# Performance work log

Measured on AMD Instinct MI355X. Metric: run time of the kernel, lower is better.

The kernel has to match this reference:

```python
import jax, jax.numpy as jnp
import numpy as np

B, T, C, H = 2, 4096, 512, 8
HD = C // H  # head_dim = 64


def setup_inputs() -> dict:
    key = jax.random.key(0)
    ks = jax.random.split(key, 5)
    s = 0.02
    return {
        "x": jax.random.normal(ks[0], (B, T, C), dtype=jnp.float32),
        "Wqkv": jax.random.normal(ks[1], (C, 3 * C), dtype=jnp.float32) * s,
        "bqkv": jax.random.normal(ks[2], (3 * C,), dtype=jnp.float32) * s,
        "Wproj": jax.random.normal(ks[3], (C, C), dtype=jnp.float32) * s,
        "bproj": jax.random.normal(ks[4], (C,), dtype=jnp.float32) * s,
    }


def reference(x, Wqkv, bqkv, Wproj, bproj):
    b, t, c = x.shape
    qkv = x @ Wqkv + bqkv                      # [B,T,3C]
    q, k, v = jnp.split(qkv, 3, axis=-1)
    # [B,T,C] -> [B,H,T,HD]
    q = q.reshape(b, t, H, HD).transpose(0, 2, 1, 3)
    k = k.reshape(b, t, H, HD).transpose(0, 2, 1, 3)
    v = v.reshape(b, t, H, HD).transpose(0, 2, 1, 3)
    att = jnp.einsum("bhqd,bhkd->bhqk", q, k) / jnp.sqrt(jnp.float32(HD))
    causal = jnp.tril(jnp.ones((t, t), dtype=bool))
    att = jnp.where(causal, att, -jnp.inf)
    att = jax.nn.softmax(att, axis=-1)
    y = jnp.einsum("bhqk,bhkd->bhqd", att, v)  # [B,H,T,HD]
    y = y.transpose(0, 2, 1, 3).reshape(b, t, c)
    return y @ Wproj + bproj
```

## Files before the change

kernel.cpp:

```cpp
#include <hip/hip_runtime.h>
#include <math.h>

#define NB 2
#define NT 4096
#define NC 512
#define NH 8
#define ND 64
#define N3C (3*NC)

typedef __attribute__((ext_vector_type(8))) __bf16 bf16x8;
typedef __attribute__((ext_vector_type(4))) __bf16 bf16x4;
typedef __attribute__((ext_vector_type(4))) float  f32x4;

__device__ __forceinline__ void load_lds16(const __bf16* g, __bf16* l) {
    __builtin_amdgcn_global_load_lds(
        (const __attribute__((address_space(1))) void*)g,
        (__attribute__((address_space(3))) void*)l, 16, 0, 0);
}

__global__ __launch_bounds__(256) void cvt_bf16_kernel(
    const float* __restrict__ x, __bf16* __restrict__ xb, int n)
{
    const int i = (blockIdx.x * 256 + threadIdx.x) << 3;
    if (i < n) {
        float4 a = *(const float4*)(x + i);
        float4 b = *(const float4*)(x + i + 4);
        bf16x8 o;
        o[0] = (__bf16)a.x; o[1] = (__bf16)a.y; o[2] = (__bf16)a.z; o[3] = (__bf16)a.w;
        o[4] = (__bf16)b.x; o[5] = (__bf16)b.y; o[6] = (__bf16)b.z; o[7] = (__bf16)b.w;
        *(bf16x8*)(xb + i) = o;
    }
}

__global__ __launch_bounds__(256) void prep_kernel(
    const float* __restrict__ Wqkv, const float* __restrict__ Wproj,
    __bf16* __restrict__ wqkvt, __bf16* __restrict__ wprojt)
{
    __shared__ float T[64][65];
    int id = blockIdx.x;
    const float* W; __bf16* Wt; int N, n0, k0;
    if (id < 192) { W = Wqkv;  Wt = wqkvt;  N = N3C; n0 = (id % 24) << 6; k0 = (id / 24) << 6; }
    else { id -= 192; W = Wproj; Wt = wprojt; N = NC;  n0 = (id & 7) << 6;  k0 = (id >> 3) << 6; }
    const int K = NC;

    const int tx = threadIdx.x & 15, ty = threadIdx.x >> 4;
#pragma unroll
    for (int i = 0; i < 4; ++i) {
        const int r = ty + (i << 4);
        float4 v = *(const float4*)(W + (size_t)(k0 + r) * N + n0 + (tx << 2));
        T[r][(tx << 2) + 0] = v.x;
        T[r][(tx << 2) + 1] = v.y;
        T[r][(tx << 2) + 2] = v.z;
        T[r][(tx << 2) + 3] = v.w;
    }
    __syncthreads();
#pragma unroll
    for (int i = 0; i < 4; ++i) {
        const int nr = ty + (i << 4);
        bf16x4 o;
        o[0] = (__bf16)T[(tx << 2) + 0][nr];
        o[1] = (__bf16)T[(tx << 2) + 1][nr];
        o[2] = (__bf16)T[(tx << 2) + 2][nr];
        o[3] = (__bf16)T[(tx << 2) + 3][nr];
        *(bf16x4*)(Wt + (size_t)(n0 + nr) * K + k0 + (tx << 2)) = o;
    }
}

template<int BM>
__global__ __launch_bounds__(256) void gemm_glds_kernel(
    const __bf16* __restrict__ A, const __bf16* __restrict__ Bt,
    const float* __restrict__ bias, void* __restrict__ Cout,
    int M, int N, int K, int out_bf16)
{
    constexpr int IT = BM / 32;
    constexpr int AI = BM / 32;
    __shared__ __align__(16) __bf16 As[BM * 64];
    __shared__ __align__(16) __bf16 Bs[128 * 64];

    const int tid  = threadIdx.x;
    const int w    = tid >> 6, lane = tid & 63;
    const int g    = lane >> 4, n = lane & 15;
    const int n7   = n & 7;
    const int wr   = (w >> 1) * (BM / 2);
    const int wc   = (w & 1) << 6;
    const int m0   = blockIdx.y * BM, n0 = blockIdx.x << 7;

    const __bf16* ag[AI]; __bf16* al[AI];
#pragma unroll
    for (int q = 0; q < AI; ++q) {
        const int G = w * (BM * 2) + q * 64 + lane;
        const int r = G >> 3, pg = G & 7, kg = pg ^ (r & 7);
        ag[q] = A + (size_t)(m0 + r) * K + (kg << 3);
        al[q] = As + ((w * (BM * 2) + q * 64) << 3);
    }
    const __bf16* bg[4]; __bf16* bl[4];
#pragma unroll
    for (int q = 0; q < 4; ++q) {
        const int G = w * 256 + q * 64 + lane;
        const int r = G >> 3, pg = G & 7, kg = pg ^ (r & 7);
        bg[q] = Bt + (size_t)(n0 + r) * K + (kg << 3);
        bl[q] = Bs + ((w * 256 + q * 64) << 3);
    }

    f32x4 acc[IT][4];
#pragma unroll
    for (int i = 0; i < IT; ++i)
#pragma unroll
        for (int j = 0; j < 4; ++j) acc[i][j] = (f32x4){0.f, 0.f, 0.f, 0.f};

    const int ksteps = K >> 6;
    for (int ks = 0; ks < ksteps; ++ks) {
        __syncthreads();
        const int ko = ks << 6;
#pragma unroll
        for (int q = 0; q < AI; ++q) load_lds16(ag[q] + ko, al[q]);
#pragma unroll
        for (int q = 0; q < 4;  ++q) load_lds16(bg[q] + ko, bl[q]);
        __syncthreads();

#pragma unroll
        for (int s = 0; s < 2; ++s) {
            bf16x8 af[IT], bf[4];
#pragma unroll
            for (int i = 0; i < IT; ++i) {
                const int row = wr + (i << 4) + n;
                af[i] = *(const bf16x8*)&As[(row << 6) + ((((s << 2) + g) ^ n7) << 3)];
            }
#pragma unroll
            for (int j = 0; j < 4; ++j) {
                const int row = wc + (j << 4) + n;
                bf[j] = *(const bf16x8*)&Bs[(row << 6) + ((((s << 2) + g) ^ n7) << 3)];
            }
#pragma unroll
            for (int i = 0; i < IT; ++i)
#pragma unroll
                for (int j = 0; j < 4; ++j)
                    acc[i][j] = __builtin_amdgcn_mfma_f32_16x16x32_bf16(af[i], bf[j], acc[i][j], 0, 0, 0);
        }
    }

#pragma unroll
    for (int j = 0; j < 4; ++j) {
        const int colg = n0 + wc + (j << 4) + n;
        const float bb = bias[colg];
#pragma unroll
        for (int i = 0; i < IT; ++i) {
#pragma unroll
            for (int reg = 0; reg < 4; ++reg) {
                const int rowg = m0 + wr + (i << 4) + (g << 2) + reg;
                const float v = acc[i][j][reg] + bb;
                if (out_bf16)
                    ((__bf16*)Cout)[(size_t)rowg * N + colg] = (__bf16)v;
                else
                    ((float*)Cout)[(size_t)rowg * N + colg] = v;
            }
        }
    }
}

__global__ __launch_bounds__(512) void attn_kernel(
    const __bf16* __restrict__ qkv, __bf16* __restrict__ out)
{
    __shared__ __align__(16) unsigned char SMEM[36864];
    __bf16 (*QPs)[72] = (__bf16(*)[72])SMEM;
    __bf16 (*Ks)[72]  = (__bf16(*)[72])(SMEM + 18432);
    __bf16 (*Vt)[72]  = (__bf16(*)[72])(SMEM + 27648);

    const int tid  = threadIdx.x;
    const int xi   = blockIdx.x;
    const int bh   = blockIdx.y;
    const int qb   = (bh < 8) ? (31 - xi) : xi;
    const int b    = bh >> 3, h = bh & 7;
    const int qr0  = qb << 7;
    const size_t base = (size_t)b * NT * N3C;
    const int col  = h * ND;

    const int w    = tid >> 6;
    const int lane = tid & 63;
    const int g    = lane >> 4;
    const int n    = lane & 15;
    const int qg   = w >> 1;
    const int kh   = w & 1;
    const int qrow0 = qg << 5;
    const int kcol0 = kh << 5;
    const int sw   = (g ^ (n >> 2)) << 3;

    const int kr = tid >> 3;
    const int kc = (tid & 7) << 3;
    const int vd = lane;
    const int vk = w << 2;

    const __bf16* kptr = qkv + base + NC + col + kc;
    const __bf16* vptr = qkv + base + 2 * NC + col + vd;

#pragma unroll
    for (int i = 0; i < 2; ++i) {
        const int r = kr + (i << 6);
        bf16x8 v = *(const bf16x8*)(qkv + base + (size_t)(qr0 + r) * N3C + col + kc);
        bf16x8 q;
#pragma unroll
        for (int j = 0; j < 8; ++j) q[j] = (__bf16)(0.125f * (float)v[j]);
        *(bf16x8*)&QPs[r][kc] = q;
    }
    __syncthreads();

    bf16x8 qf[2][2];
#pragma unroll
    for (int qt = 0; qt < 2; ++qt)
#pragma unroll
        for (int hh = 0; hh < 2; ++hh)
            qf[qt][hh] = *(const bf16x8*)&QPs[qrow0 + (qt << 4) + n][(hh << 5) + (g << 3)];

    bf16x8 ones;
#pragma unroll
    for (int j = 0; j < 8; ++j) ones[j] = (__bf16)1.0f;

    f32x4 O[2][4];
#pragma unroll
    for (int qt = 0; qt < 2; ++qt)
#pragma unroll
        for (int dt = 0; dt < 4; ++dt) O[qt][dt] = (f32x4){0.f, 0.f, 0.f, 0.f};
    f32x4 L[2] = {{0.f,0.f,0.f,0.f},{0.f,0.f,0.f,0.f}};

    bf16x8 kreg = *(const bf16x8*)(kptr + (size_t)kr * N3C);
    __bf16 vreg[8];
#pragma unroll
    for (int j = 0; j < 4; ++j) {
        vreg[j]     = vptr[(size_t)(vk + j) * N3C];
        vreg[4 + j] = vptr[(size_t)(vk + 32 + j) * N3C];
    }

    const int ntiles = (qb << 1) + 2;
    for (int jt = 0; jt < ntiles; ++jt) {
        __syncthreads();
        *(bf16x8*)&Ks[kr][kc] = kreg;
        {
            bf16x4 va, vb;
#pragma unroll
            for (int j = 0; j < 4; ++j) { va[j] = vreg[j]; vb[j] = vreg[4 + j]; }
            *(bf16x4*)&Vt[vd][vk]      = va;
            *(bf16x4*)&Vt[vd][vk + 32] = vb;
        }
        __syncthreads();

        if (jt + 1 < ntiles) {
            const int kr1 = (jt + 1) << 6;
            kreg = *(const bf16x8*)(kptr + (size_t)(kr1 + kr) * N3C);
#pragma unroll
            for (int j = 0; j < 4; ++j) {
                vreg[j]     = vptr[(size_t)(kr1 + vk + j) * N3C];
                vreg[4 + j] = vptr[(size_t)(kr1 + vk + 32 + j) * N3C];
            }
        }

        f32x4 S[2][2];
        __builtin_amdgcn_s_setprio(1);
#pragma unroll
        for (int t = 0; t < 2; ++t) {
            const bf16x8 k0 = *(const bf16x8*)&Ks[kcol0 + (t << 4) + n][(g << 3)];
            const bf16x8 k1 = *(const bf16x8*)&Ks[kcol0 + (t << 4) + n][32 + (g << 3)];
#pragma unroll
            for (int qt = 0; qt < 2; ++qt) {
                f32x4 a = {0.f, 0.f, 0.f, 0.f};
                a = __builtin_amdgcn_mfma_f32_16x16x32_bf16(qf[qt][0], k0, a, 0, 0, 0);
                a = __builtin_amdgcn_mfma_f32_16x16x32_bf16(qf[qt][1], k1, a, 0, 0, 0);
                S[qt][t] = a;
            }
        }
        __builtin_amdgcn_s_setprio(0);

        if (jt >= (qb << 1)) {
#pragma unroll
            for (int qt = 0; qt < 2; ++qt)
#pragma unroll
                for (int t = 0; t < 2; ++t)
#pragma unroll
                    for (int reg = 0; reg < 4; ++reg) {
                        const int kg = (jt << 6) + kcol0 + (t << 4) + n;
                        const int qgl = qr0 + qrow0 + (qt << 4) + (g << 2) + reg;
                        if (kg > qgl) S[qt][t][reg] = -INFINITY;
                    }
        }

#pragma unroll
        for (int qt = 0; qt < 2; ++qt)
#pragma unroll
            for (int t = 0; t < 2; ++t)
#pragma unroll
                for (int reg = 0; reg < 4; ++reg)
                    QPs[qrow0 + (qt << 4) + (g << 2) + reg]
                       [kcol0 + (((t << 4) + n) ^ (g << 3))] =
                        (__bf16)__expf(S[qt][t][reg]);

        bf16x8 vf[4];
#pragma unroll
        for (int dt = 0; dt < 4; ++dt) {
            const int vr = (dt << 4) + n;
            vf[dt] = *(const bf16x8*)&Vt[vr][kcol0 + (g << 3)];
        }

        __builtin_amdgcn_s_setprio(1);
#pragma unroll
        for (int qt = 0; qt < 2; ++qt) {
            const bf16x8 p = *(const bf16x8*)&QPs[qrow0 + (qt << 4) + n][kcol0 + sw];
            L[qt] = __builtin_amdgcn_mfma_f32_16x16x32_bf16(p, ones, L[qt], 0, 0, 0);
#pragma unroll
            for (int dt = 0; dt < 4; ++dt)
                O[qt][dt] = __builtin_amdgcn_mfma_f32_16x16x32_bf16(p, vf[dt], O[qt][dt], 0, 0, 0);
        }
        __builtin_amdgcn_s_setprio(0);
    }

    __syncthreads();
    float* red = (float*)SMEM;
    if (kh == 1) {
#pragma unroll
        for (int qt = 0; qt < 2; ++qt)
#pragma unroll
            for (int reg = 0; reg < 4; ++reg) {
                const int qlx = qrow0 + (qt << 4) + (g << 2) + reg;
#pragma unroll
                for (int dt = 0; dt < 4; ++dt)
                    red[qlx * 64 + (dt << 4) + n] = O[qt][dt][reg];
                if (n == 0) red[8192 + qlx] = L[qt][reg];
            }
    }
    __syncthreads();
    if (kh == 0) {
#pragma unroll
        for (int qt = 0; qt < 2; ++qt)
#pragma unroll
            for (int reg = 0; reg < 4; ++reg) {
                const int qlx = qrow0 + (qt << 4) + (g << 2) + reg;
                const float inv = 1.0f / (L[qt][reg] + red[8192 + qlx]);
                const size_t row = (size_t)b * NT + qr0 + qlx;
#pragma unroll
                for (int dt = 0; dt < 4; ++dt)
                    out[row * NC + col + (dt << 4) + n] =
                        (__bf16)((O[qt][dt][reg] + red[qlx * 64 + (dt << 4) + n]) * inv);
            }
    }
}

extern "C" void kernel_launch(void* const* d_in, const int* in_sizes, int n_in,
                              void* d_out, int out_size, void* d_ws, size_t ws_size,
                              hipStream_t stream)
{
    const float* x     = (const float*)d_in[0];
    const float* Wqkv  = (const float*)d_in[1];
    const float* bqkv  = (const float*)d_in[2];
    const float* Wproj = (const float*)d_in[3];
    const float* bproj = (const float*)d_in[4];
    float* out = (float*)d_out;

    char* ws = (char*)d_ws;
    __bf16* xb     = (__bf16*)(ws);
    __bf16* qkvb   = (__bf16*)(ws + 8388608);
    __bf16* attb   = (__bf16*)(ws + 33554432);
    __bf16* wqkvt  = (__bf16*)(ws + 41943040);
    __bf16* wprojt = (__bf16*)(ws + 43515904);

    cvt_bf16_kernel<<<dim3(2048), dim3(256), 0, stream>>>(x, xb, NB * NT * NC);
    prep_kernel<<<dim3(256), dim3(256), 0, stream>>>(Wqkv, Wproj, wqkvt, wprojt);

    gemm_glds_kernel<128><<<dim3(N3C / 128, (NB * NT) / 128), dim3(256), 0, stream>>>(
        xb, wqkvt, bqkv, qkvb, NB * NT, N3C, NC, 1);

    attn_kernel<<<dim3(NT / 128, NB * NH), dim3(512), 0, stream>>>(qkvb, attb);

    gemm_glds_kernel<64><<<dim3(NC / 128, (NB * NT) / 64), dim3(256), 0, stream>>>(
        attb, wprojt, bproj, out, NB * NT, NC, NC, 0);
}
```

Measured before the change: 201.7 us.

## Split causal attention KV range across blocks with partial-sum combine kernel

Adds a split-KV (flash-decoding style) path in which later query blocks divide their KV tiles among up to four workgroups. Each workgroup writes unnormalized fp32 partial outputs and row sums, and a new combine kernel adds them and normalizes. The aim is to even out the causal triangle's load imbalance and raise the grid from 512 to 1280 workgroups. In exchange it adds fp32 partial-output traffic (about 40MB of workspace) and one more kernel launch, and it falls back to the single-pass kernel when the workspace is too small.

```diff
diff --git a/kernel.cpp b/kernel.cpp
--- a/kernel.cpp
+++ b/kernel.cpp
@@ -159,7 +159,8 @@
 }
 
 __global__ __launch_bounds__(512) void attn_kernel(
-    const __bf16* __restrict__ qkv, __bf16* __restrict__ out)
+    const __bf16* __restrict__ qkv, int mono, __bf16* __restrict__ outb,
+    float* __restrict__ Opart, float* __restrict__ Lpart)
 {
     __shared__ __align__(16) unsigned char SMEM[36864];
     __bf16 (*QPs)[72] = (__bf16(*)[72])SMEM;
@@ -169,8 +170,25 @@
     const int tid  = threadIdx.x;
     const int xi   = blockIdx.x;
     const int bh   = blockIdx.y;
-    const int qb   = (bh < 8) ? (31 - xi) : xi;
     const int b    = bh >> 3, h = bh & 7;
+
+    int qb, jt0, jt1, pid;
+    if (mono) {
+        qb = (bh < 8) ? (31 - xi) : xi;
+        jt0 = 0; jt1 = (qb << 1) + 2; pid = 0;
+    } else {
+        const int a  = (xi < 8) ? 0 : ((xi < 24) ? 1 : ((xi < 48) ? 2 : 3));
+        const int np = a + 1;
+        const int off = xi - 4 * a * np;
+        qb = (a << 3) + off / np;
+        const int p  = off % np;
+        const int ntiles = (qb << 1) + 2;
+        const int chunk = ntiles / np, rem = ntiles % np;
+        jt0 = p * chunk + (p < rem ? p : rem);
+        jt1 = jt0 + chunk + (p < rem ? 1 : 0);
+        pid = bh * 80 + xi;
+    }
+
     const int qr0  = qb << 7;
     const size_t base = (size_t)b * NT * N3C;
     const int col  = h * ND;
@@ -222,16 +240,16 @@
         for (int dt = 0; dt < 4; ++dt) O[qt][dt] = (f32x4){0.f, 0.f, 0.f, 0.f};
     f32x4 L[2] = {{0.f,0.f,0.f,0.f},{0.f,0.f,0.f,0.f}};
 
-    bf16x8 kreg = *(const bf16x8*)(kptr + (size_t)kr * N3C);
+    const int r0 = jt0 << 6;
+    bf16x8 kreg = *(const bf16x8*)(kptr + (size_t)(r0 + kr) * N3C);
     __bf16 vreg[8];
 #pragma unroll
     for (int j = 0; j < 4; ++j) {
-        vreg[j]     = vptr[(size_t)(vk + j) * N3C];
-        vreg[4 + j] = vptr[(size_t)(vk + 32 + j) * N3C];
-    }
-
-    const int ntiles = (qb << 1) + 2;
-    for (int jt = 0; jt < ntiles; ++jt) {
+        vreg[j]     = vptr[(size_t)(r0 + vk + j) * N3C];
+        vreg[4 + j] = vptr[(size_t)(r0 + vk + 32 + j) * N3C];
+    }
+
+    for (int jt = jt0; jt < jt1; ++jt) {
         __syncthreads();
         *(bf16x8*)&Ks[kr][kc] = kreg;
         {
@@ -243,7 +261,7 @@
         }
         __syncthreads();
 
-        if (jt + 1 < ntiles) {
+        if (jt + 1 < jt1) {
             const int kr1 = (jt + 1) << 6;
             kreg = *(const bf16x8*)(kptr + (size_t)(kr1 + kr) * N3C);
 #pragma unroll
@@ -332,13 +350,54 @@
 #pragma unroll
             for (int reg = 0; reg < 4; ++reg) {
                 const int qlx = qrow0 + (qt << 4) + (g << 2) + reg;
-                const float inv = 1.0f / (L[qt][reg] + red[8192 + qlx]);
-                const size_t row = (size_t)b * NT + qr0 + qlx;
-#pragma unroll
-                for (int dt = 0; dt < 4; ++dt)
-                    out[row * NC + col + (dt << 4) + n] =
-                        (__bf16)((O[qt][dt][reg] + red[qlx * 64 + (dt << 4) + n]) * inv);
-            }
+                const float Ltot = L[qt][reg] + red[8192 + qlx];
+                if (mono) {
+                    const float inv = 1.0f / Ltot;
+                    const size_t row = (size_t)b * NT + qr0 + qlx;
+#pragma unroll
+                    for (int dt = 0; dt < 4; ++dt)
+                        outb[row * NC + col + (dt << 4) + n] =
+                            (__bf16)((O[qt][dt][reg] + red[qlx * 64 + (dt << 4) + n]) * inv);
+                } else {
+                    if (n == 0) Lpart[(size_t)pid * 128 + qlx] = Ltot;
+#pragma unroll
+                    for (int dt = 0; dt < 4; ++dt)
+                        Opart[(size_t)pid * 8192 + qlx * 64 + (dt << 4) + n] =
+                            O[qt][dt][reg] + red[qlx * 64 + (dt << 4) + n];
+                }
+            }
+    }
+}
+
+__global__ __launch_bounds__(256) void combine_kernel(
+    const float* __restrict__ Opart, const float* __restrict__ Lpart,
+    __bf16* __restrict__ outb)
+{
+    const int gid = blockIdx.x;
+    const int qb  = gid & 31, bh = gid >> 5;
+    const int b   = bh >> 3, h = bh & 7;
+    const int a   = qb >> 3, r7 = qb & 7;
+    const int np  = a + 1;
+    const int pbase = bh * 80 + 4 * a * np + r7 * np;
+
+    const int tid = threadIdx.x;
+    const int c   = (tid & 15) << 2;
+    const int rb  = tid >> 4;
+#pragma unroll
+    for (int pass = 0; pass < 8; ++pass) {
+        const int r = rb + (pass << 4);
+        float Ls = 0.f;
+        f32x4 acc = {0.f, 0.f, 0.f, 0.f};
+        for (int p = 0; p < np; ++p) {
+            Ls += Lpart[(size_t)(pbase + p) * 128 + r];
+            const f32x4 v = *(const f32x4*)&Opart[(size_t)(pbase + p) * 8192 + (r << 6) + c];
+            acc += v;
+        }
+        const float inv = 1.0f / Ls;
+        bf16x4 o;
+        o[0] = (__bf16)(acc[0] * inv); o[1] = (__bf16)(acc[1] * inv);
+        o[2] = (__bf16)(acc[2] * inv); o[3] = (__bf16)(acc[3] * inv);
+        *(bf16x4*)&outb[((size_t)b * NT + (qb << 7) + r) * NC + h * ND + c] = o;
     }
 }
 
@@ -359,6 +418,9 @@
     __bf16* attb   = (__bf16*)(ws + 33554432);
     __bf16* wqkvt  = (__bf16*)(ws + 41943040);
     __bf16* wprojt = (__bf16*)(ws + 43515904);
+    float*  Opart  = (float*)(ws + 44040192);
+    float*  Lpart  = (float*)(ws + 85983232);
+    const size_t SPLIT_NEED = 86638592;
 
     cvt_bf16_kernel<<<dim3(2048), dim3(256), 0, stream>>>(x, xb, NB * NT * NC);
     prep_kernel<<<dim3(256), dim3(256), 0, stream>>>(Wqkv, Wproj, wqkvt, wprojt);
@@ -366,7 +428,14 @@
     gemm_glds_kernel<128><<<dim3(N3C / 128, (NB * NT) / 128), dim3(256), 0, stream>>>(
         xb, wqkvt, bqkv, qkvb, NB * NT, N3C, NC, 1);
 
-    attn_kernel<<<dim3(NT / 128, NB * NH), dim3(512), 0, stream>>>(qkvb, attb);
+    if (ws_size >= SPLIT_NEED) {
+        attn_kernel<<<dim3(80, NB * NH), dim3(512), 0, stream>>>(
+            qkvb, 0, attb, Opart, Lpart);
+        combine_kernel<<<dim3(512), dim3(256), 0, stream>>>(Opart, Lpart, attb);
+    } else {
+        attn_kernel<<<dim3(NT / 128, NB * NH), dim3(512), 0, stream>>>(
+            qkvb, 1, attb, (float*)nullptr, (float*)nullptr);
+    }
 
     gemm_glds_kernel<64><<<dim3(NC / 128, (NB * NT) / 64), dim3(256), 0, stream>>>(
         attb, wprojt, bproj, out, NB * NT, NC, NC, 0);
```

Result: no change. 204.0 us (+1.1%).

## Shrink attention blocks to 64 query rows with async double-buffered K loads

Applied to the files above, without the earlier changes.

Attention blocks now cover 64 query rows with 256 threads instead of 128 rows with 512, so the grid has twice as many blocks and finer causal load balance. K tiles are loaded straight into an XOR-swizzled, double-buffered LDS region with global_load_lds instead of passing through registers. The exponential becomes a hardware exp2 with log2(e) folded into the Q scale, and the causal mask is applied only on the diagonal tile. Costs are more blocks and repeated setup per block, and a V path that still goes through registers.

```diff
diff --git a/kernel.cpp b/kernel.cpp
--- a/kernel.cpp
+++ b/kernel.cpp
@@ -16,6 +16,10 @@
     __builtin_amdgcn_global_load_lds(
         (const __attribute__((address_space(1))) void*)g,
         (__attribute__((address_space(3))) void*)l, 16, 0, 0);
+}
+
+__device__ __forceinline__ float exp2_fast(float x) {
+    return __builtin_amdgcn_exp2f(x);
 }
 
 __global__ __launch_bounds__(256) void cvt_bf16_kernel(
@@ -158,20 +162,22 @@
     }
 }
 
-__global__ __launch_bounds__(512) void attn_kernel(
+__global__ __launch_bounds__(256, 4) void attn_kernel(
     const __bf16* __restrict__ qkv, __bf16* __restrict__ out)
 {
-    __shared__ __align__(16) unsigned char SMEM[36864];
+    __shared__ __align__(16) unsigned char SMEM[34816];
     __bf16 (*QPs)[72] = (__bf16(*)[72])SMEM;
-    __bf16 (*Ks)[72]  = (__bf16(*)[72])(SMEM + 18432);
-    __bf16 (*Vt)[72]  = (__bf16(*)[72])(SMEM + 27648);
+    __bf16* Ks        = (__bf16*)(SMEM + 9216);
+    __bf16 (*Vt)[72]  = (__bf16(*)[72])(SMEM + 25600);
 
     const int tid  = threadIdx.x;
     const int xi   = blockIdx.x;
     const int bh   = blockIdx.y;
-    const int qb   = (bh < 8) ? (31 - xi) : xi;
     const int b    = bh >> 3, h = bh & 7;
-    const int qr0  = qb << 7;
+    const int m    = (bh < 8) ? (63 - xi) : xi;
+    const int jt1  = m + 1;
+
+    const int qr0  = m << 6;
     const size_t base = (size_t)b * NT * N3C;
     const int col  = h * ND;
 
@@ -188,19 +194,35 @@
     const int kr = tid >> 3;
     const int kc = (tid & 7) << 3;
     const int vd = lane;
-    const int vk = w << 2;
-
-    const __bf16* kptr = qkv + base + NC + col + kc;
+    const int vk = w << 3;
+
+    const __bf16* kg_src[2]; __bf16* kl_dst[2];
+#pragma unroll
+    for (int q = 0; q < 2; ++q) {
+        const int G = w * 128 + q * 64 + lane;
+        const int r = G >> 3, pg = G & 7, kgr = pg ^ (r & 7);
+        kg_src[q] = qkv + base + NC + col + (size_t)r * N3C + (kgr << 3);
+        kl_dst[q] = Ks + ((w * 128 + q * 64) << 3);
+    }
     const __bf16* vptr = qkv + base + 2 * NC + col + vd;
 
 #pragma unroll
     for (int i = 0; i < 2; ++i) {
-        const int r = kr + (i << 6);
+        const int r = kr + (i << 5);
         bf16x8 v = *(const bf16x8*)(qkv + base + (size_t)(qr0 + r) * N3C + col + kc);
         bf16x8 q;
 #pragma unroll
-        for (int j = 0; j < 8; ++j) q[j] = (__bf16)(0.125f * (float)v[j]);
+        for (int j = 0; j < 8; ++j) q[j] = (__bf16)(0.18033688f * (float)v[j]);
         *(bf16x8*)&QPs[r][kc] = q;
+    }
+
+#pragma unroll
+    for (int q = 0; q < 2; ++q) load_lds16(kg_src[q], kl_dst[q]);
+    __bf16 vreg[16];
+#pragma unroll
+    for (int j = 0; j < 8; ++j) {
+        vreg[j]     = vptr[(size_t)(vk + j) * N3C];
+        vreg[8 + j] = vptr[(size_t)(vk + 32 + j) * N3C];
     }
     __syncthreads();
 
@@ -222,43 +244,39 @@
         for (int dt = 0; dt < 4; ++dt) O[qt][dt] = (f32x4){0.f, 0.f, 0.f, 0.f};
     f32x4 L[2] = {{0.f,0.f,0.f,0.f},{0.f,0.f,0.f,0.f}};
 
-    bf16x8 kreg = *(const bf16x8*)(kptr + (size_t)kr * N3C);
-    __bf16 vreg[8];
-#pragma unroll
-    for (int j = 0; j < 4; ++j) {
-        vreg[j]     = vptr[(size_t)(vk + j) * N3C];
-        vreg[4 + j] = vptr[(size_t)(vk + 32 + j) * N3C];
-    }
-
-    const int ntiles = (qb << 1) + 2;
-    for (int jt = 0; jt < ntiles; ++jt) {
+    for (int jt = 0; jt < jt1; ++jt) {
         __syncthreads();
-        *(bf16x8*)&Ks[kr][kc] = kreg;
         {
-            bf16x4 va, vb;
-#pragma unroll
-            for (int j = 0; j < 4; ++j) { va[j] = vreg[j]; vb[j] = vreg[4 + j]; }
-            *(bf16x4*)&Vt[vd][vk]      = va;
-            *(bf16x4*)&Vt[vd][vk + 32] = vb;
+            bf16x8 va, vb;
+#pragma unroll
+            for (int j = 0; j < 8; ++j) { va[j] = vreg[j]; vb[j] = vreg[8 + j]; }
+            *(bf16x8*)&Vt[vd][vk]      = va;
+            *(bf16x8*)&Vt[vd][vk + 32] = vb;
         }
         __syncthreads();
 
-        if (jt + 1 < ntiles) {
+        if (jt + 1 < jt1) {
+            const size_t roff = (size_t)((jt + 1) << 6) * N3C;
+            const int bo = ((jt + 1) & 1) << 12;
+#pragma unroll
+            for (int q = 0; q < 2; ++q) load_lds16(kg_src[q] + roff, kl_dst[q] + bo);
             const int kr1 = (jt + 1) << 6;
-            kreg = *(const bf16x8*)(kptr + (size_t)(kr1 + kr) * N3C);
-#pragma unroll
-            for (int j = 0; j < 4; ++j) {
+#pragma unroll
+            for (int j = 0; j < 8; ++j) {
                 vreg[j]     = vptr[(size_t)(kr1 + vk + j) * N3C];
-                vreg[4 + j] = vptr[(size_t)(kr1 + vk + 32 + j) * N3C];
-            }
-        }
-
+                vreg[8 + j] = vptr[(size_t)(kr1 + vk + 32 + j) * N3C];
+            }
+        }
+
+        const __bf16* kb = Ks + ((jt & 1) << 12);
         f32x4 S[2][2];
         __builtin_amdgcn_s_setprio(1);
 #pragma unroll
         for (int t = 0; t < 2; ++t) {
-            const bf16x8 k0 = *(const bf16x8*)&Ks[kcol0 + (t << 4) + n][(g << 3)];
-            const bf16x8 k1 = *(const bf16x8*)&Ks[kcol0 + (t << 4) + n][32 + (g << 3)];
+            const int row = kcol0 + (t << 4) + n;
+            const int r7  = row & 7;
+            const bf16x8 k0 = *(const bf16x8*)&kb[(row << 6) + ((g ^ r7) << 3)];
+            const bf16x8 k1 = *(const bf16x8*)&kb[(row << 6) + (((g ^ 4) ^ r7) << 3)];
 #pragma unroll
             for (int qt = 0; qt < 2; ++qt) {
                 f32x4 a = {0.f, 0.f, 0.f, 0.f};
@@ -269,14 +287,14 @@
         }
         __builtin_amdgcn_s_setprio(0);
 
-        if (jt >= (qb << 1)) {
+        if (jt == m) {
 #pragma unroll
             for (int qt = 0; qt < 2; ++qt)
 #pragma unroll
                 for (int t = 0; t < 2; ++t)
 #pragma unroll
                     for (int reg = 0; reg < 4; ++reg) {
-                        const int kg = (jt << 6) + kcol0 + (t << 4) + n;
+                        const int kg  = (jt << 6) + kcol0 + (t << 4) + n;
                         const int qgl = qr0 + qrow0 + (qt << 4) + (g << 2) + reg;
                         if (kg > qgl) S[qt][t][reg] = -INFINITY;
                     }
@@ -290,7 +308,7 @@
                 for (int reg = 0; reg < 4; ++reg)
                     QPs[qrow0 + (qt << 4) + (g << 2) + reg]
                        [kcol0 + (((t << 4) + n) ^ (g << 3))] =
-                        (__bf16)__expf(S[qt][t][reg]);
+                        (__bf16)exp2_fast(S[qt][t][reg]);
 
         bf16x8 vf[4];
 #pragma unroll
@@ -322,7 +340,7 @@
 #pragma unroll
                 for (int dt = 0; dt < 4; ++dt)
                     red[qlx * 64 + (dt << 4) + n] = O[qt][dt][reg];
-                if (n == 0) red[8192 + qlx] = L[qt][reg];
+                if (n == 0) red[4096 + qlx] = L[qt][reg];
             }
     }
     __syncthreads();
@@ -332,7 +350,7 @@
 #pragma unroll
             for (int reg = 0; reg < 4; ++reg) {
                 const int qlx = qrow0 + (qt << 4) + (g << 2) + reg;
-                const float inv = 1.0f / (L[qt][reg] + red[8192 + qlx]);
+                const float inv = 1.0f / (L[qt][reg] + red[4096 + qlx]);
                 const size_t row = (size_t)b * NT + qr0 + qlx;
 #pragma unroll
                 for (int dt = 0; dt < 4; ++dt)
@@ -366,7 +384,7 @@
     gemm_glds_kernel<128><<<dim3(N3C / 128, (NB * NT) / 128), dim3(256), 0, stream>>>(
         xb, wqkvt, bqkv, qkvb, NB * NT, N3C, NC, 1);
 
-    attn_kernel<<<dim3(NT / 128, NB * NH), dim3(512), 0, stream>>>(qkvb, attb);
+    attn_kernel<<<dim3(64, NB * NH), dim3(256), 0, stream>>>(qkvb, attb);
 
     gemm_glds_kernel<64><<<dim3(NC / 128, (NB * NT) / 64), dim3(256), 0, stream>>>(
         attb, wprojt, bproj, out, NB * NT, NC, NC, 0);
```

Result: no change. 205.7 us (+2.0%).
